# Performance work log

Measured on AMD Instinct MI355X. Metric: run time of the kernel, lower is better.

## Reference

```python
import jax, jax.numpy as jnp
import numpy as np

EPS = 1e-12  # F.normalize default eps


def _l2_normalize(x):
    n = jnp.linalg.norm(x, axis=-1, keepdims=True)
    return x / jnp.maximum(n, EPS)


def setup_inputs() -> dict:
    key = jax.random.key(0)
    k1, k2 = jax.random.split(key)
    B, N, D = 2048, 100000, 256
    query = jax.random.normal(k1, (B, D), dtype=jnp.float32)
    memory_states = jax.random.normal(k2, (N, D), dtype=jnp.float32)
    return {"query": query, "memory_states": memory_states, "k": 8}


def reference(query, memory_states, k):
    # cosine-similarity retrieval: normalize both sides, dense matmul, top-k, gather
    mem_norm = _l2_normalize(memory_states)          # [N, D]
    query_norm = _l2_normalize(query)                # [B, D]
    scores = query_norm @ mem_norm.T                 # [B, N]
    top_k_scores, indices = jax.lax.top_k(scores, k)  # [B, k] each
    retrieved = memory_states[indices]               # [B, k, D] (raw, un-normalized states as in torch)
    return retrieved, top_k_scores
```

## Files before the change

### kernel.cpp

```cpp
#include <hip/hip_runtime.h>
#include <hip/hip_bf16.h>
#include <stdint.h>

#define DIM 256
#define TOPK 8
#define NSTRIPS 64
#define STRIP_TOP 8
#define QT 256
#define NT 64
#define CAND (NSTRIPS * STRIP_TOP)
#define RESCORE 64
#define SLOTS 33
#define IDXMASK 0x1FFFFu

typedef __attribute__((ext_vector_type(8))) short short8;
typedef __attribute__((ext_vector_type(4))) float floatx4;
typedef __attribute__((address_space(3))) unsigned int lds_u32;
typedef __attribute__((address_space(1))) const unsigned int gbl_u32;

__device__ __forceinline__ unsigned short f2bf(float f) {
    union { float f; uint32_t u; } v; v.f = f;
    uint32_t u = v.u;
    uint32_t r = u + 0x7fffu + ((u >> 16) & 1u);
    return (unsigned short)(r >> 16);
}

__device__ __forceinline__ uint32_t umaxu(uint32_t a, uint32_t b) { return a > b ? a : b; }
__device__ __forceinline__ uint32_t uminu(uint32_t a, uint32_t b) { return a < b ? a : b; }

__device__ __forceinline__ uint32_t mono16(float f) {
    uint32_t u = __float_as_uint(f);
    uint32_t m = u ^ ((uint32_t)(((int32_t)u) >> 31) | 0x80000000u);
    return m >> 16;
}

__global__ void prep_kernel(const float* __restrict__ query,
                            const float* __restrict__ mem,
                            float* __restrict__ rnorm_mem,
                            unsigned short* __restrict__ q_bf16,
                            unsigned short* __restrict__ mem_bf16,
                            int B, int N)
{
    int wave = threadIdx.x >> 6;
    int lane = threadIdx.x & 63;
    int row  = blockIdx.x * 4 + wave;
    int total = N + B;
    if (row >= total) return;
    const float* src = (row < N) ? (mem + (size_t)row * DIM)
                                 : (query + (size_t)(row - N) * DIM);
    float4 v = ((const float4*)src)[lane];
    float ss = v.x * v.x + v.y * v.y + v.z * v.z + v.w * v.w;
#pragma unroll
    for (int m = 32; m >= 1; m >>= 1) ss += __shfl_xor(ss, m, 64);
    float rinv = 1.0f / fmaxf(sqrtf(ss), 1e-12f);
    ushort4 o;
    o.x = f2bf(v.x * rinv); o.y = f2bf(v.y * rinv);
    o.z = f2bf(v.z * rinv); o.w = f2bf(v.w * rinv);
    if (row < N) {
        if (lane == 0) rnorm_mem[row] = rinv;
        if (mem_bf16) ((ushort4*)(mem_bf16 + (size_t)row * DIM))[lane] = o;
    } else {
        ((ushort4*)(q_bf16 + (size_t)(row - N) * DIM))[lane] = o;
    }
}

template<bool PRE>
__global__ __launch_bounds__(256, 2) void score_select_kernel(
    const float* __restrict__ mem,
    const float* __restrict__ rnorm_mem,
    const unsigned short* __restrict__ mem_bf16,
    const unsigned short* __restrict__ q_bf16,
    uint32_t* __restrict__ cand_key,
    int B, int N)
{
    __shared__ unsigned short lds_m[NT * DIM];
    __shared__ uint32_t lds_s[QT * SLOTS];

    const int t    = threadIdx.x;
    const int wave = t >> 6;
    const int lane = t & 63;
    const int quad = lane >> 4;
    const int l16  = lane & 15;

    const int qbase = blockIdx.x * QT;
    const int strip = blockIdx.y;
    const int SS    = (N + NSTRIPS - 1) / NSTRIPS;
    const int n0    = strip * SS;
    const int nend  = (n0 + SS < N) ? (n0 + SS) : N;
    const int limit = nend - n0;
    const int ntiles = (limit + NT - 1) / NT;

    short8 afrag[4][8];
#pragma unroll
    for (int s = 0; s < 4; s++) {
        int qrow = qbase + s * 64 + wave * 16 + l16;
        const unsigned short* qp = q_bf16 + (size_t)qrow * DIM + quad * 8;
#pragma unroll
        for (int ks = 0; ks < 8; ks++)
            afrag[s][ks] = *(const short8*)(qp + ks * 32);
    }

    uint32_t ts[STRIP_TOP];
#pragma unroll
    for (int j = 0; j < STRIP_TOP; j++) ts[j] = 0;

    const int l5  = lane >> 5;
    const int s32 = lane & 31;

    auto stage = [&](int tileIdx) {
        int base = n0 + tileIdx * NT;
        if (PRE) {
#pragma unroll
            for (int is = 0; is < 8; is++) {
                int rl = is * 8 + wave * 2 + l5;
                int n = base + rl; if (n >= nend) n = nend - 1;
                int chunk = s32 ^ (rl & 7);
                const unsigned short* gp = mem_bf16 + (size_t)n * DIM + chunk * 8;
                unsigned short* lp = lds_m + (is * 8 + wave * 2) * DIM;
                __builtin_amdgcn_global_load_lds((gbl_u32*)(const void*)gp,
                                                 (lds_u32*)(void*)lp, 16, 0, 0);
            }
        } else {
#pragma unroll 4
            for (int i = 0; i < 16; i++) {
                int rl = i * 4 + wave;
                int n = base + rl;
                ushort4 o;
                if (n < nend) {
                    float rinv = rnorm_mem[n];
                    float4 v = ((const float4*)(mem + (size_t)n * DIM))[lane];
                    o.x = f2bf(v.x * rinv); o.y = f2bf(v.y * rinv);
                    o.z = f2bf(v.z * rinv); o.w = f2bf(v.w * rinv);
                } else { o.x = 0; o.y = 0; o.z = 0; o.w = 0; }
                int slot = (lane >> 1) ^ (rl & 7);
                *(ushort4*)(lds_m + rl * DIM + slot * 8 + (lane & 1) * 4) = o;
            }
        }
    };

    stage(0);
    __syncthreads();

    const floatx4 zero4 = {0.f, 0.f, 0.f, 0.f};
    for (int tile = 0; tile < ntiles; tile++) {
        floatx4 acc[4][4];
#pragma unroll
        for (int s = 0; s < 4; s++)
#pragma unroll
            for (int nt = 0; nt < 4; nt++) acc[s][nt] = zero4;

#pragma unroll
        for (int ks = 0; ks < 8; ks++) {
#pragma unroll
            for (int nt = 0; nt < 4; nt++) {
                int row = nt * 16 + l16;
                int slot = (ks * 4 + quad) ^ (l16 & 7);
                short8 b = *(const short8*)(lds_m + row * DIM + slot * 8);
#pragma unroll
                for (int s = 0; s < 4; s++)
                    acc[s][nt] = __builtin_amdgcn_mfma_f32_16x16x32_bf16(afrag[s][ks], b, acc[s][nt], 0, 0, 0);
            }
        }
#pragma unroll
        for (int s = 0; s < 4; s++) {
            int qrow = s * 64 + wave * 16 + quad * 4;
#pragma unroll
            for (int r = 0; r < 4; r++) {
                uint32_t p02 = mono16(acc[s][0][r]) | (mono16(acc[s][2][r]) << 16);
                uint32_t p13 = mono16(acc[s][1][r]) | (mono16(acc[s][3][r]) << 16);
                lds_s[(qrow + r) * SLOTS + l16]      = p02;
                lds_s[(qrow + r) * SLOTS + 16 + l16] = p13;
            }
        }
        __syncthreads();

        if (tile + 1 < ntiles) stage(tile + 1);

        const int tloc = tile * NT;
        const uint4* sp = (const uint4*)(lds_s + t * SLOTS);
        bool full = (tloc + NT <= limit);
#pragma unroll
        for (int j4 = 0; j4 < 8; j4++) {
            uint4 v4 = sp[j4];
#pragma unroll
            for (int e = 0; e < 4; e++) {
                uint32_t v = (e == 0) ? v4.x : (e == 1) ? v4.y : (e == 2) ? v4.z : v4.w;
                int j = j4 * 4 + e;
                uint32_t key_lo = (v << 16) | (uint32_t)(tloc + j);
                uint32_t key_hi = (v & 0xFFFF0000u) | (uint32_t)(tloc + j + 32);
                if (!full) {
                    if (tloc + j >= limit)      key_lo = 0;
                    if (tloc + j + 32 >= limit) key_hi = 0;
                }
                if (key_lo > ts[0]) {
#pragma unroll
                    for (int j2 = 0; j2 < STRIP_TOP - 1; j2++)
                        ts[j2] = uminu(umaxu(ts[j2], key_lo), ts[j2 + 1]);
                    ts[STRIP_TOP - 1] = umaxu(ts[STRIP_TOP - 1], key_lo);
                }
                if (key_hi > ts[0]) {
#pragma unroll
                    for (int j2 = 0; j2 < STRIP_TOP - 1; j2++)
                        ts[j2] = uminu(umaxu(ts[j2], key_hi), ts[j2 + 1]);
                    ts[STRIP_TOP - 1] = umaxu(ts[STRIP_TOP - 1], key_hi);
                }
            }
        }
        __syncthreads();
    }

    size_t off = ((size_t)(qbase + t) * NSTRIPS + strip) * STRIP_TOP;
#pragma unroll
    for (int j = 0; j < STRIP_TOP; j++) {
        uint32_t k = ts[j];
        uint32_t loc = k & 0xFFFFu;
        uint32_t key2 = ((k >> 17) << 17) | (uint32_t)(n0 + (int)loc);
        cand_key[off + j] = key2;
    }
}

__global__ __launch_bounds__(256) void rescore_kernel(
    const float* __restrict__ query,
    const float* __restrict__ mem,
    const uint32_t* __restrict__ cand_key,
    float* __restrict__ out,
    int B, int N)
{
    __shared__ uint32_t cs[CAND];
    __shared__ float  lds_q[DIM];
    __shared__ double red[4];
    __shared__ double qss_sh;
    __shared__ int    sel_i[RESCORE];
    __shared__ double rs[RESCORE];
    __shared__ double best_s[TOPK];
    __shared__ int    best_i[TOPK];

    const int t    = threadIdx.x;
    const int q    = blockIdx.x;
    const int lane = t & 63;
    const int wave = t >> 6;

    for (int i = t; i < CAND; i += 256)
        cs[i] = cand_key[(size_t)q * CAND + i];

    float qv = query[(size_t)q * DIM + t];
    lds_q[t] = qv;
    double p = (double)qv * (double)qv;
#pragma unroll
    for (int m = 32; m >= 1; m >>= 1) p += __shfl_xor(p, m, 64);
    if (lane == 0) red[wave] = p;
    __syncthreads();
    if (t == 0) qss_sh = red[0] + red[1] + red[2] + red[3];

    {
        uint32_t* qcs = cs + wave * 128;
        for (int k = 2; k <= 128; k <<= 1) {
            for (int j = k >> 1; j > 0; j >>= 1) {
                int i  = 2 * lane - (lane & (j - 1));
                int ip = i + j;
                bool up = ((i & k) == 0);
                uint32_t a = qcs[i], b2 = qcs[ip];
                bool aFirst = a > b2;
                bool doSwap = up ? (!aFirst) : aFirst;
                if (doSwap) { qcs[i] = b2; qcs[ip] = a; }
            }
        }
        if (lane < 16) sel_i[wave * 16 + lane] = (int)(qcs[lane] & IDXMASK);
    }
    __syncthreads();

    double qss = qss_sh;
    for (int r = 0; r < 16; r++) {
        int c = wave * 16 + r;
        int idx = sel_i[c];
        float4 mv = ((const float4*)(mem + (size_t)idx * DIM))[lane];
        float4 qv4 = ((const float4*)lds_q)[lane];
        double dqm = (double)mv.x * (double)qv4.x + (double)mv.y * (double)qv4.y
                   + (double)mv.z * (double)qv4.z + (double)mv.w * (double)qv4.w;
        double dmm = (double)mv.x * (double)mv.x + (double)mv.y * (double)mv.y
                   + (double)mv.z * (double)mv.z + (double)mv.w * (double)mv.w;
#pragma unroll
        for (int m = 32; m >= 1; m >>= 1) {
            dqm += __shfl_xor(dqm, m, 64);
            dmm += __shfl_xor(dmm, m, 64);
        }
        if (lane == 0)
            rs[c] = dqm / (fmax(sqrt(qss), 1e-12) * fmax(sqrt(dmm), 1e-12));
    }
    __syncthreads();

    if (t == 0) {
        double bs[TOPK]; int bi[TOPK];
        for (int i = 0; i < TOPK; i++) { bs[i] = -1e300; bi[i] = 0x7fffffff; }
        for (int c = 0; c < RESCORE; c++) {
            double s = rs[c]; int id = sel_i[c];
            bool better = (s > bs[TOPK - 1]) || (s == bs[TOPK - 1] && id < bi[TOPK - 1]);
            if (better) {
                int pos = TOPK - 1;
                while (pos > 0) {
                    bool b2 = (s > bs[pos - 1]) || (s == bs[pos - 1] && id < bi[pos - 1]);
                    if (!b2) break;
                    bs[pos] = bs[pos - 1]; bi[pos] = bi[pos - 1]; pos--;
                }
                bs[pos] = s; bi[pos] = id;
            }
        }
        for (int i = 0; i < TOPK; i++) { best_s[i] = bs[i]; best_i[i] = bi[i]; }
    }
    __syncthreads();

    size_t score_base = (size_t)B * TOPK * DIM;
    if (t < TOPK) out[score_base + (size_t)q * TOPK + t] = (float)best_s[t];

#pragma unroll
    for (int rep = 0; rep < 2; rep++) {
        int j  = t >> 5;
        int d4 = (t & 31) + rep * 32;
        int idx = best_i[j];
        float4 v = ((const float4*)(mem + (size_t)idx * DIM))[d4];
        ((float4*)(out + ((size_t)q * TOPK + j) * DIM))[d4] = v;
    }
}

extern "C" void kernel_launch(void* const* d_in, const int* in_sizes, int n_in,
                              void* d_out, int out_size, void* d_ws, size_t ws_size,
                              hipStream_t stream)
{
    const float* query = (const float*)d_in[0];
    const float* mem   = (const float*)d_in[1];
    int B = in_sizes[0] / DIM;
    int N = in_sizes[1] / DIM;

    auto align256 = [](size_t x) { return (x + 255) & ~(size_t)255; };
    size_t off = 0;
    auto alloc = [&](size_t bytes) { void* p = (char*)d_ws + off; off += align256(bytes); return p; };

    float* rnorm_mem       = (float*)alloc((size_t)N * 4);
    unsigned short* q_bf16 = (unsigned short*)alloc((size_t)B * DIM * 2);
    uint32_t* cand_key     = (uint32_t*)alloc((size_t)B * CAND * 4);
    size_t base_need = off;
    unsigned short* mem_bf16 = (unsigned short*)((char*)d_ws + base_need);
    bool pre = (base_need + align256((size_t)N * DIM * 2)) <= ws_size;
    if (!pre) mem_bf16 = nullptr;

    int prep_blocks = (N + B + 3) / 4;
    prep_kernel<<<prep_blocks, 256, 0, stream>>>(query, mem, rnorm_mem, q_bf16,
                                                 mem_bf16, B, N);

    dim3 g2((B + QT - 1) / QT, NSTRIPS);
    if (pre)
        score_select_kernel<true><<<g2, 256, 0, stream>>>(mem, rnorm_mem, mem_bf16, q_bf16,
                                                          cand_key, B, N);
    else
        score_select_kernel<false><<<g2, 256, 0, stream>>>(mem, rnorm_mem, mem_bf16, q_bf16,
                                                           cand_key, B, N);

    rescore_kernel<<<B, 256, 0, stream>>>(query, mem, cand_key, (float*)d_out, B, N);
}
```

Before: 421.1 us.

## Bias scores by one to drop sign handling and use med3 top-8 insertion

Accumulators now start at 1.0, so cosine scores land in roughly [0,2] and are non-negative after clamping. That lets the raw float bits serve as monotone keys instead of the sign-flip mono16 transform. The strip top-8 insertion now uses a single v_med3_u32 per step, and each pair of keys is inserted max-first under wave-uniform __any branches, which avoids divergent per-lane branching. This depends on the +1 bias keeping the ordering intact, and clamping at zero merges scores just below -1 with -1.

```diff
diff --git a/kernel.cpp b/kernel.cpp
--- a/kernel.cpp
+++ b/kernel.cpp
@@ -28,10 +28,14 @@
 __device__ __forceinline__ uint32_t umaxu(uint32_t a, uint32_t b) { return a > b ? a : b; }
 __device__ __forceinline__ uint32_t uminu(uint32_t a, uint32_t b) { return a < b ? a : b; }
 
-__device__ __forceinline__ uint32_t mono16(float f) {
-    uint32_t u = __float_as_uint(f);
-    uint32_t m = u ^ ((uint32_t)(((int32_t)u) >> 31) | 0x80000000u);
-    return m >> 16;
+__device__ __forceinline__ void top8_insert(uint32_t* ts, uint32_t key) {
+#pragma unroll
+    for (int j = 0; j < STRIP_TOP - 1; j++) {
+        uint32_t m;
+        asm("v_med3_u32 %0, %1, %2, %3" : "=v"(m) : "v"(ts[j]), "v"(ts[j + 1]), "v"(key));
+        ts[j] = m;
+    }
+    ts[STRIP_TOP - 1] = umaxu(ts[STRIP_TOP - 1], key);
 }
 
 __global__ void prep_kernel(const float* __restrict__ query,
@@ -141,13 +145,13 @@
     stage(0);
     __syncthreads();
 
-    const floatx4 zero4 = {0.f, 0.f, 0.f, 0.f};
+    const floatx4 one4 = {1.f, 1.f, 1.f, 1.f};
     for (int tile = 0; tile < ntiles; tile++) {
         floatx4 acc[4][4];
 #pragma unroll
         for (int s = 0; s < 4; s++)
 #pragma unroll
-            for (int nt = 0; nt < 4; nt++) acc[s][nt] = zero4;
+            for (int nt = 0; nt < 4; nt++) acc[s][nt] = one4;
 
 #pragma unroll
         for (int ks = 0; ks < 8; ks++) {
@@ -166,10 +170,12 @@
             int qrow = s * 64 + wave * 16 + quad * 4;
 #pragma unroll
             for (int r = 0; r < 4; r++) {
-                uint32_t p02 = mono16(acc[s][0][r]) | (mono16(acc[s][2][r]) << 16);
-                uint32_t p13 = mono16(acc[s][1][r]) | (mono16(acc[s][3][r]) << 16);
-                lds_s[(qrow + r) * SLOTS + l16]      = p02;
-                lds_s[(qrow + r) * SLOTS + 16 + l16] = p13;
+                uint32_t u0 = __float_as_uint(fmaxf(acc[s][0][r], 0.f));
+                uint32_t u1 = __float_as_uint(fmaxf(acc[s][1][r], 0.f));
+                uint32_t u2 = __float_as_uint(fmaxf(acc[s][2][r], 0.f));
+                uint32_t u3 = __float_as_uint(fmaxf(acc[s][3][r], 0.f));
+                lds_s[(qrow + r) * SLOTS + l16]      = (u2 & 0xFFFF0000u) | (u0 >> 16);
+                lds_s[(qrow + r) * SLOTS + 16 + l16] = (u3 & 0xFFFF0000u) | (u1 >> 16);
             }
         }
         __syncthreads();
@@ -192,17 +198,12 @@
                     if (tloc + j >= limit)      key_lo = 0;
                     if (tloc + j + 32 >= limit) key_hi = 0;
                 }
-                if (key_lo > ts[0]) {
-#pragma unroll
-                    for (int j2 = 0; j2 < STRIP_TOP - 1; j2++)
-                        ts[j2] = uminu(umaxu(ts[j2], key_lo), ts[j2 + 1]);
-                    ts[STRIP_TOP - 1] = umaxu(ts[STRIP_TOP - 1], key_lo);
-                }
-                if (key_hi > ts[0]) {
-#pragma unroll
-                    for (int j2 = 0; j2 < STRIP_TOP - 1; j2++)
-                        ts[j2] = uminu(umaxu(ts[j2], key_hi), ts[j2 + 1]);
-                    ts[STRIP_TOP - 1] = umaxu(ts[STRIP_TOP - 1], key_hi);
+                uint32_t kmax = umaxu(key_lo, key_hi);
+                uint32_t kmin = uminu(key_lo, key_hi);
+                if (__any(kmax > ts[0])) {
+                    top8_insert(ts, kmax);
+                    if (__any(kmin > ts[0]))
+                        top8_insert(ts, kmin);
                 }
             }
         }
```

Result: faster. 412.4 us (-2.1%).
